# Kernel tuning notes

Measured on AMD Instinct MI355X. Metric: run time of the kernel, lower is better.

The kernel has to match this reference:

```python
import jax, jax.numpy as jnp
import numpy as np

COMMITMENT_COST = 0.25
NUM_EMBEDDINGS = 8192
EMBEDDING_DIM = 256


def setup_inputs() -> dict:
    key = jax.random.key(0)
    k1, k2 = jax.random.split(key)
    inputs = jax.random.normal(k1, (32, 256, EMBEDDING_DIM), dtype=jnp.float32)
    codebook = jax.random.normal(k2, (NUM_EMBEDDINGS, EMBEDDING_DIM), dtype=jnp.float32)
    # match nn.Embedding init: N(0,1) then L2-normalize rows
    codebook = codebook / jnp.linalg.norm(codebook, axis=1, keepdims=True)
    return {"inputs": inputs, "codebook": codebook}


def reference(inputs, codebook):
    B, K, D = inputs.shape
    flat = inputs.reshape(-1, D).astype(jnp.float32)  # [N, D], N = B*K
    N = flat.shape[0]

    distances = (
        jnp.sum(flat * flat, axis=1, keepdims=True)
        + jnp.sum(codebook * codebook, axis=1)
        - 2.0 * flat @ codebook.T
    )
    indices = jnp.argmin(distances, axis=1)  # [N]

    # codebook lookup (equivalent to one-hot @ codebook)
    quantized = codebook[indices].reshape(B, K, D)

    e_latent_loss = jnp.mean((jax.lax.stop_gradient(quantized) - inputs) ** 2)
    q_latent_loss = jnp.mean((quantized - jax.lax.stop_gradient(inputs)) ** 2)
    loss = q_latent_loss + COMMITMENT_COST * e_latent_loss

    # straight-through estimator
    quantized_ste = inputs + jax.lax.stop_gradient(quantized - inputs)

    # perplexity from codebook usage histogram (== mean of one-hot encodings)
    counts = jnp.zeros((NUM_EMBEDDINGS,), dtype=jnp.float32).at[indices].add(1.0)
    avg_probs = counts / N
    perplexity = jnp.exp(-jnp.sum(avg_probs * jnp.log(avg_probs + 1e-10)))

    return quantized_ste, loss, perplexity
```

## Files before the change

### kernel.cpp

```cpp
#include <hip/hip_runtime.h>
#include <math.h>

#define NTOK 8192
#define NEMB 8192
#define DIM  256

typedef _Float16 f16x8 __attribute__((ext_vector_type(8)));
typedef _Float16 f16x4 __attribute__((ext_vector_type(4)));
typedef float    f32x4 __attribute__((ext_vector_type(4)));

__global__ __launch_bounds__(256) void convert_kernel(
        const float* __restrict__ X, const float* __restrict__ C,
        _Float16* __restrict__ Xh, _Float16* __restrict__ Ch,
        float* __restrict__ cnorm, float* __restrict__ xnorm,
        unsigned long long* __restrict__ keys, int* __restrict__ counts) {
    const bool isC = (blockIdx.y != 0);
    if (isC && blockIdx.x < 8) {
        ((int4*)counts)[blockIdx.x * 256 + threadIdx.x] = make_int4(0, 0, 0, 0);
    }
    if (!isC && blockIdx.x < 8) {
        int4 ff = make_int4(-1, -1, -1, -1);
        ((int4*)keys)[blockIdx.x * 512 + threadIdx.x * 2]     = ff;
        ((int4*)keys)[blockIdx.x * 512 + threadIdx.x * 2 + 1] = ff;
    }
    const float* src = isC ? C : X;
    _Float16* dst = isC ? Ch : Xh;
    size_t t = (size_t)blockIdx.x * 256 + threadIdx.x;
    float4 x = *(const float4*)&src[t * 4];
    f16x4 h;
    h[0] = (_Float16)x.x; h[1] = (_Float16)x.y;
    h[2] = (_Float16)x.z; h[3] = (_Float16)x.w;
    *(f16x4*)&dst[t * 4] = h;
    float s = x.x * x.x + x.y * x.y + x.z * x.z + x.w * x.w;
    #pragma unroll
    for (int off = 32; off >= 1; off >>= 1) s += __shfl_xor(s, off);
    if ((threadIdx.x & 63) == 0) {
        if (isC) cnorm[t >> 6] = s; else xnorm[t >> 6] = s;
    }
}

__device__ __forceinline__ int swz(int row) { return (row + (row >> 2)) & 3; }

__device__ __forceinline__ void stage_pair32(
        const _Float16* __restrict__ Ag, const _Float16* __restrict__ Bg,
        _Float16* pair, int t) {
    #pragma unroll
    for (int c = 0; c < 2; ++c) {
        int gr  = c * 256 + t;
        int row = gr >> 2;
        int kg  = (gr & 3) ^ swz(row);
        __builtin_amdgcn_global_load_lds(
            (const __attribute__((address_space(1))) void*)(Ag + (size_t)row * DIM + kg * 8),
            (__attribute__((address_space(3))) void*)(pair + (size_t)gr * 8), 16, 0, 0);
        __builtin_amdgcn_global_load_lds(
            (const __attribute__((address_space(1))) void*)(Bg + (size_t)row * DIM + kg * 8),
            (__attribute__((address_space(3))) void*)(pair + 4096 + (size_t)gr * 8), 16, 0, 0);
    }
}

__device__ __forceinline__ void compute_pair32(
        const _Float16* pair, f32x4 (&acc)[4][4],
        int wm, int wn, int lrow, int g) {
    const _Float16* Abase = pair;
    const _Float16* Bbase = pair + 4096;
    f16x8 af[4], bf_[4];
    #pragma unroll
    for (int tm = 0; tm < 4; ++tm) {
        int row = wm + tm * 16 + lrow;
        af[tm] = *(const f16x8*)&Abase[(row * 4 + (g ^ swz(row))) * 8];
    }
    #pragma unroll
    for (int tn = 0; tn < 4; ++tn) {
        int row = wn + tn * 16 + lrow;
        bf_[tn] = *(const f16x8*)&Bbase[(row * 4 + (g ^ swz(row))) * 8];
    }
    #pragma unroll
    for (int tm = 0; tm < 4; ++tm)
        #pragma unroll
        for (int tn = 0; tn < 4; ++tn)
            acc[tm][tn] = __builtin_amdgcn_mfma_f32_16x16x32_f16(
                af[tm], bf_[tn], acc[tm][tn], 0, 0, 0);
}

__global__ __launch_bounds__(256) void mfma_argmin_kernel(
        const _Float16* __restrict__ Xh, const _Float16* __restrict__ Ch,
        const float* __restrict__ cnorm,
        unsigned long long* __restrict__ keys) {
    __shared__ __align__(16) _Float16 lds[16384];

    const int t = threadIdx.x;
    const int wid = t >> 6, lane = t & 63;
    const int tb0 = blockIdx.x * 128;
    const int cb0 = blockIdx.y * 128;
    const int wm = (wid >> 1) * 64;
    const int wn = (wid & 1) * 64;
    const int lrow = lane & 15;
    const int g = lane >> 4;

    float cn[16];
    #pragma unroll
    for (int tm = 0; tm < 4; ++tm)
        #pragma unroll
        for (int reg = 0; reg < 4; ++reg)
            cn[tm * 4 + reg] = cnorm[cb0 + wm + tm * 16 + g * 4 + reg];

    f32x4 acc[4][4];
    #pragma unroll
    for (int a = 0; a < 4; ++a)
        #pragma unroll
        for (int b = 0; b < 4; ++b) acc[a][b] = (f32x4)0.0f;

    const _Float16* Ag = Ch + (size_t)cb0 * DIM;
    const _Float16* Bg = Xh + (size_t)tb0 * DIM;

    stage_pair32(Ag, Bg, lds, t);
    __syncthreads();
    #pragma unroll
    for (int p = 0; p < 8; ++p) {
        _Float16* cur = lds + (p & 1) * 8192;
        if (p < 7) {
            _Float16* nxt = lds + ((p + 1) & 1) * 8192;
            stage_pair32(Ag + (p + 1) * 32, Bg + (p + 1) * 32, nxt, t);
        }
        compute_pair32(cur, acc, wm, wn, lrow, g);
        __syncthreads();
    }

    float* cmb_v = (float*)lds;
    int*   cmb_i = (int*)((float*)lds + 256);

    #pragma unroll
    for (int tn = 0; tn < 4; ++tn) {
        float bv = 1e30f; int bi = 0x7fffffff;
        #pragma unroll
        for (int tm = 0; tm < 4; ++tm) {
            #pragma unroll
            for (int reg = 0; reg < 4; ++reg) {
                float d = fmaf(-2.0f, acc[tm][tn][reg], cn[tm * 4 + reg]);
                int code = cb0 + wm + tm * 16 + g * 4 + reg;
                if (d < bv) { bv = d; bi = code; }
            }
        }
        #pragma unroll
        for (int off = 16; off <= 32; off <<= 1) {
            float ov = __shfl_xor(bv, off);
            int   oi = __shfl_xor(bi, off);
            if (ov < bv || (ov == bv && oi < bi)) { bv = ov; bi = oi; }
        }
        if (g == 0) {
            int tl = wn + tn * 16 + lrow;
            cmb_v[tl * 2 + (wid >> 1)] = bv;
            cmb_i[tl * 2 + (wid >> 1)] = bi;
        }
    }
    __syncthreads();
    if (t < 128) {
        float v0 = cmb_v[t * 2], v1 = cmb_v[t * 2 + 1];
        int   i0 = cmb_i[t * 2], i1 = cmb_i[t * 2 + 1];
        bool tk = (v1 < v0) || (v1 == v0 && i1 < i0);
        float bv = tk ? v1 : v0;
        int   bi = tk ? i1 : i0;
        unsigned long long key =
            ((unsigned long long)__builtin_bit_cast(unsigned, bv + 64.0f) << 32)
            | (unsigned)bi;
        atomicMin(&keys[tb0 + t], key);
    }
}

__global__ __launch_bounds__(256) void gather_kernel(
        const float* __restrict__ C, const unsigned long long* __restrict__ keys,
        const float* __restrict__ xnorm, int* __restrict__ counts,
        float* __restrict__ out, float* __restrict__ psum) {
    __shared__ int idx_lds[32];
    const int m0 = blockIdx.x * 32;
    const int t = threadIdx.x;
    if (t < 32) {
        unsigned long long k = keys[m0 + t];
        int bi  = (int)(unsigned)k;
        float d = __builtin_bit_cast(float, (unsigned)(k >> 32)) - 64.0f;
        idx_lds[t] = bi;
        atomicAdd(&counts[bi], 1);
        float lt = d + xnorm[m0 + t];
        #pragma unroll
        for (int off = 1; off < 32; off <<= 1) lt += __shfl_xor(lt, off);
        if (t == 0) psum[blockIdx.x] = lt;
    }
    __syncthreads();
    const int wid = t >> 6, lane = t & 63;
    #pragma unroll
    for (int r = 0; r < 8; ++r) {
        int token = m0 + wid * 8 + r;
        int e = idx_lds[wid * 8 + r];
        float4 q = *(const float4*)&C[(size_t)e * DIM + lane * 4];
        *(float4*)&out[(size_t)token * DIM + lane * 4] = q;
    }
}

__global__ __launch_bounds__(256) void finalize_kernel(
        const int* __restrict__ counts, const float* __restrict__ psum,
        float* __restrict__ out) {
    const int t = threadIdx.x;
    double local = 0.0;
    #pragma unroll 1
    for (int e = t; e < NEMB; e += 256) {
        float p = (float)counts[e] * (1.0f / (float)NTOK);
        local += (double)(p * logf(p + 1e-10f));
    }
    float ls = psum[t];
    #pragma unroll
    for (int off = 32; off >= 1; off >>= 1) {
        local += __shfl_xor(local, off);
        ls    += __shfl_xor(ls, off);
    }
    __shared__ double she[4];
    __shared__ float  shs[4];
    int lane = t & 63, wid = t >> 6;
    if (lane == 0) { she[wid] = local; shs[wid] = ls; }
    __syncthreads();
    if (t == 0) {
        double ent = she[0] + she[1] + she[2] + she[3];
        float  ssq = shs[0] + shs[1] + shs[2] + shs[3];
        out[(size_t)NTOK * DIM]     = 1.25f * ssq / (float)((size_t)NTOK * DIM);
        out[(size_t)NTOK * DIM + 1] = expf((float)(-ent));
    }
}

extern "C" void kernel_launch(void* const* d_in, const int* in_sizes, int n_in,
                              void* d_out, int out_size, void* d_ws, size_t ws_size,
                              hipStream_t stream) {
    const float* X = (const float*)d_in[0];
    const float* C = (const float*)d_in[1];
    float* out = (float*)d_out;

    char* ws = (char*)d_ws;
    size_t o = 0;
    _Float16* Xh = (_Float16*)(ws + o); o += (size_t)NTOK * DIM * 2;
    _Float16* Ch = (_Float16*)(ws + o); o += (size_t)NEMB * DIM * 2;
    float* cnorm = (float*)(ws + o); o += (size_t)NEMB * 4;
    float* xnorm = (float*)(ws + o); o += (size_t)NTOK * 4;
    unsigned long long* keys = (unsigned long long*)(ws + o); o += (size_t)NTOK * 8;
    int* counts  = (int*)(ws + o);   o += (size_t)NEMB * 4;
    float* psum  = (float*)(ws + o);

    convert_kernel<<<dim3(NTOK * DIM / 4 / 256, 2), 256, 0, stream>>>(
        X, C, Xh, Ch, cnorm, xnorm, keys, counts);
    mfma_argmin_kernel<<<dim3(NTOK / 128, NEMB / 128), 256, 0, stream>>>(
        Xh, Ch, cnorm, keys);
    gather_kernel<<<256, 256, 0, stream>>>(
        C, keys, xnorm, counts, out, psum);
    finalize_kernel<<<1, 256, 0, stream>>>(counts, psum, out);
}
```

Baseline: 132.9 us.

## Enlarge argmin GEMM tile to 256x128 with explicit vmcnt-pipelined staging

Doubles the codebook dimension of each workgroup tile to 256 codes, so each wave computes an 8x4 grid of MFMA tiles and global-to-LDS traffic per FLOP drops. The double-buffered loop is rewritten with explicit s_waitcnt vmcnt and raw barriers instead of __syncthreads, and MFMA issue priority is raised with s_setprio. This raises register and LDS use per block (launch bounds target 2 blocks/CU) and halves the grid size, which may reduce occupancy and latency hiding.

```diff
diff --git a/kernel.cpp b/kernel.cpp
--- a/kernel.cpp
+++ b/kernel.cpp
@@ -41,91 +41,110 @@
 
 __device__ __forceinline__ int swz(int row) { return (row + (row >> 2)) & 3; }
 
-__device__ __forceinline__ void stage_pair32(
+template<int N>
+__device__ __forceinline__ void wait_vmcnt() {
+    asm volatile("s_waitcnt vmcnt(%0)" :: "n"(N) : "memory");
+}
+
+__device__ __forceinline__ void stage_k32(
         const _Float16* __restrict__ Ag, const _Float16* __restrict__ Bg,
-        _Float16* pair, int t) {
+        _Float16* buf, int t) {
+    #pragma unroll
+    for (int c = 0; c < 4; ++c) {
+        int gr  = c * 256 + t;
+        int row = gr >> 2;
+        int kg  = (gr & 3) ^ swz(row);
+        __builtin_amdgcn_global_load_lds(
+            (const __attribute__((address_space(1))) void*)(Ag + (size_t)row * DIM + kg * 8),
+            (__attribute__((address_space(3))) void*)(buf + (size_t)gr * 8), 16, 0, 0);
+    }
     #pragma unroll
     for (int c = 0; c < 2; ++c) {
         int gr  = c * 256 + t;
         int row = gr >> 2;
         int kg  = (gr & 3) ^ swz(row);
         __builtin_amdgcn_global_load_lds(
-            (const __attribute__((address_space(1))) void*)(Ag + (size_t)row * DIM + kg * 8),
-            (__attribute__((address_space(3))) void*)(pair + (size_t)gr * 8), 16, 0, 0);
-        __builtin_amdgcn_global_load_lds(
             (const __attribute__((address_space(1))) void*)(Bg + (size_t)row * DIM + kg * 8),
-            (__attribute__((address_space(3))) void*)(pair + 4096 + (size_t)gr * 8), 16, 0, 0);
-    }
-}
-
-__device__ __forceinline__ void compute_pair32(
-        const _Float16* pair, f32x4 (&acc)[4][4],
+            (__attribute__((address_space(3))) void*)(buf + 8192 + (size_t)gr * 8), 16, 0, 0);
+    }
+}
+
+__device__ __forceinline__ void compute_k32(
+        const _Float16* buf, f32x4 (&acc)[8][4],
         int wm, int wn, int lrow, int g) {
-    const _Float16* Abase = pair;
-    const _Float16* Bbase = pair + 4096;
-    f16x8 af[4], bf_[4];
-    #pragma unroll
-    for (int tm = 0; tm < 4; ++tm) {
+    const _Float16* Ab = buf;
+    const _Float16* Bb = buf + 8192;
+    f16x8 af[8], bf_[4];
+    #pragma unroll
+    for (int tm = 0; tm < 8; ++tm) {
         int row = wm + tm * 16 + lrow;
-        af[tm] = *(const f16x8*)&Abase[(row * 4 + (g ^ swz(row))) * 8];
+        af[tm] = *(const f16x8*)&Ab[(row * 4 + (g ^ swz(row))) * 8];
     }
     #pragma unroll
     for (int tn = 0; tn < 4; ++tn) {
         int row = wn + tn * 16 + lrow;
-        bf_[tn] = *(const f16x8*)&Bbase[(row * 4 + (g ^ swz(row))) * 8];
-    }
-    #pragma unroll
-    for (int tm = 0; tm < 4; ++tm)
+        bf_[tn] = *(const f16x8*)&Bb[(row * 4 + (g ^ swz(row))) * 8];
+    }
+    __builtin_amdgcn_s_setprio(1);
+    #pragma unroll
+    for (int tm = 0; tm < 8; ++tm)
         #pragma unroll
         for (int tn = 0; tn < 4; ++tn)
             acc[tm][tn] = __builtin_amdgcn_mfma_f32_16x16x32_f16(
                 af[tm], bf_[tn], acc[tm][tn], 0, 0, 0);
-}
-
-__global__ __launch_bounds__(256) void mfma_argmin_kernel(
+    __builtin_amdgcn_s_setprio(0);
+}
+
+__global__ __launch_bounds__(256, 2) void mfma_argmin_kernel(
         const _Float16* __restrict__ Xh, const _Float16* __restrict__ Ch,
         const float* __restrict__ cnorm,
         unsigned long long* __restrict__ keys) {
-    __shared__ __align__(16) _Float16 lds[16384];
+    __shared__ __align__(16) _Float16 lds[24576];
 
     const int t = threadIdx.x;
     const int wid = t >> 6, lane = t & 63;
     const int tb0 = blockIdx.x * 128;
-    const int cb0 = blockIdx.y * 128;
-    const int wm = (wid >> 1) * 64;
+    const int cb0 = blockIdx.y * 256;
+    const int wm = (wid >> 1) * 128;
     const int wn = (wid & 1) * 64;
     const int lrow = lane & 15;
     const int g = lane >> 4;
 
-    float cn[16];
-    #pragma unroll
-    for (int tm = 0; tm < 4; ++tm)
+    f32x4 acc[8][4];
+    #pragma unroll
+    for (int a = 0; a < 8; ++a)
+        #pragma unroll
+        for (int b = 0; b < 4; ++b) acc[a][b] = (f32x4)0.0f;
+
+    const _Float16* Ag = Ch + (size_t)cb0 * DIM;
+    const _Float16* Bg = Xh + (size_t)tb0 * DIM;
+
+    stage_k32(Ag, Bg, lds, t);
+
+#define PHASE(P, LAST)                                                        \
+    do {                                                                      \
+        if (!(LAST))                                                          \
+            stage_k32(Ag + ((P) + 1) * 32, Bg + ((P) + 1) * 32,               \
+                      lds + (((P) + 1) & 1) * 12288, t);                      \
+        wait_vmcnt<(LAST) ? 0 : 6>();                                         \
+        __builtin_amdgcn_s_barrier();                                         \
+        __builtin_amdgcn_sched_barrier(0);                                    \
+        compute_k32(lds + ((P) & 1) * 12288, acc, wm, wn, lrow, g);           \
+        __builtin_amdgcn_sched_barrier(0);                                    \
+        __builtin_amdgcn_s_barrier();                                         \
+    } while (0)
+
+    PHASE(0, false); PHASE(1, false); PHASE(2, false); PHASE(3, false);
+    PHASE(4, false); PHASE(5, false); PHASE(6, false); PHASE(7, true);
+#undef PHASE
+
+    float cn[32];
+    #pragma unroll
+    for (int tm = 0; tm < 8; ++tm)
         #pragma unroll
         for (int reg = 0; reg < 4; ++reg)
             cn[tm * 4 + reg] = cnorm[cb0 + wm + tm * 16 + g * 4 + reg];
 
-    f32x4 acc[4][4];
-    #pragma unroll
-    for (int a = 0; a < 4; ++a)
-        #pragma unroll
-        for (int b = 0; b < 4; ++b) acc[a][b] = (f32x4)0.0f;
-
-    const _Float16* Ag = Ch + (size_t)cb0 * DIM;
-    const _Float16* Bg = Xh + (size_t)tb0 * DIM;
-
-    stage_pair32(Ag, Bg, lds, t);
-    __syncthreads();
-    #pragma unroll
-    for (int p = 0; p < 8; ++p) {
-        _Float16* cur = lds + (p & 1) * 8192;
-        if (p < 7) {
-            _Float16* nxt = lds + ((p + 1) & 1) * 8192;
-            stage_pair32(Ag + (p + 1) * 32, Bg + (p + 1) * 32, nxt, t);
-        }
-        compute_pair32(cur, acc, wm, wn, lrow, g);
-        __syncthreads();
-    }
-
     float* cmb_v = (float*)lds;
     int*   cmb_i = (int*)((float*)lds + 256);
 
@@ -133,7 +152,7 @@
     for (int tn = 0; tn < 4; ++tn) {
         float bv = 1e30f; int bi = 0x7fffffff;
         #pragma unroll
-        for (int tm = 0; tm < 4; ++tm) {
+        for (int tm = 0; tm < 8; ++tm) {
             #pragma unroll
             for (int reg = 0; reg < 4; ++reg) {
                 float d = fmaf(-2.0f, acc[tm][tn][reg], cn[tm * 4 + reg]);
@@ -244,7 +263,7 @@
 
     convert_kernel<<<dim3(NTOK * DIM / 4 / 256, 2), 256, 0, stream>>>(
         X, C, Xh, Ch, cnorm, xnorm, keys, counts);
-    mfma_argmin_kernel<<<dim3(NTOK / 128, NEMB / 128), 256, 0, stream>>>(
+    mfma_argmin_kernel<<<dim3(NTOK / 128, NEMB / 256), 256, 0, stream>>>(
         Xh, Ch, cnorm, keys);
     gather_kernel<<<256, 256, 0, stream>>>(
         C, keys, xnorm, counts, out, psum);
```

Result: faster. 127.9 us (-3.7%).
